# Kernel optimization log

Measured on AMD Instinct MI355X. Metric: run time of the kernel, lower is better.

## Reference

```python
import jax, jax.numpy as jnp
import numpy as np

NUM_EMBEDDINGS = 1024
EMBEDDING_DIM = 256
COMMITMENT_COST = 0.25


def setup_inputs() -> dict:
    key = jax.random.key(0)
    k1, k2 = jax.random.split(key)
    inputs = jax.random.normal(k1, (65536, EMBEDDING_DIM), dtype=jnp.float32)
    # original init: uniform(-1/K, 1/K)
    embeddings = jax.random.uniform(
        k2, (NUM_EMBEDDINGS, EMBEDDING_DIM), dtype=jnp.float32,
        minval=-1.0 / NUM_EMBEDDINGS, maxval=1.0 / NUM_EMBEDDINGS)
    return {"inputs": inputs, "embeddings": embeddings}


def reference(inputs, embeddings):
    D = embeddings.shape[1]
    flat = inputs.reshape(-1, D)                                   # [N, D]
    distances = (jnp.sum(flat ** 2, axis=1, keepdims=True)
                 + jnp.sum(embeddings ** 2, axis=1)
                 - 2.0 * flat @ embeddings.T)
    indices = jnp.argmin(distances, axis=1)                        # [N]
    # one-hot @ codebook == direct gather
    quantized = embeddings[indices].reshape(inputs.shape)
    q_loss = jnp.mean((jax.lax.stop_gradient(quantized) - inputs) ** 2)
    e_loss = jnp.mean((quantized - jax.lax.stop_gradient(inputs)) ** 2)
    loss = q_loss + COMMITMENT_COST * e_loss
    # straight-through estimator
    quantized = inputs + jax.lax.stop_gradient(quantized - inputs)
    return quantized, loss
```

## Files before the change

### kernel.cpp

```cpp
#include <hip/hip_runtime.h>
#include <stdint.h>

#define N_ROWS 65536
#define K_CODES 1024
#define DIM 256

typedef unsigned int uint;
typedef unsigned short ushort;

#define WS_LOSS_OFF  0
#define WS_ENORM_OFF 4096
#define WS_E8_OFF    8192

typedef __attribute__((ext_vector_type(4))) float f32x4;
typedef __attribute__((ext_vector_type(4))) int   i32x4;
typedef __attribute__((ext_vector_type(8))) int   i32x8;

#define XSCALE 16.0f
#define ESCALE 256.0f
#define SCORE_C 4.8828125e-4f
#define SCALE1 0x7F7F7F7Fu

__device__ __forceinline__ uint pack4_fp8(float a, float b, float c, float d) {
    uint r = 0;
    r = __builtin_amdgcn_cvt_pk_fp8_f32(a, b, r, false);
    r = __builtin_amdgcn_cvt_pk_fp8_f32(c, d, r, true);
    return r;
}
__device__ __forceinline__ void gload_lds16(const void* g, void* l) {
    __builtin_amdgcn_global_load_lds(
        (const __attribute__((address_space(1))) void*)g,
        (__attribute__((address_space(3))) void*)l, 16, 0, 0);
}

__global__ __launch_bounds__(256) void vq_prep(const float* __restrict__ E,
                                               unsigned char* __restrict__ E8,
                                               float* __restrict__ enorm) {
    int id = blockIdx.x * 256 + threadIdx.x;
    int code = id >> 6, c4 = id & 63;
    float4 v = *reinterpret_cast<const float4*>(E + (size_t)code * DIM + c4 * 4);
    uint p = pack4_fp8(v.x * ESCALE, v.y * ESCALE, v.z * ESCALE, v.w * ESCALE);
    *reinterpret_cast<uint*>(E8 + (size_t)code * 256 + c4 * 4) = p;

    float s = v.x * v.x + v.y * v.y + v.z * v.z + v.w * v.w;
    #pragma unroll
    for (int m = 32; m >= 1; m >>= 1) s += __shfl_down(s, m, 64);
    if (c4 == 0) enorm[code] = s;
}

__global__ __launch_bounds__(256, 2) void vq_main(const float* __restrict__ X,
                                                  const unsigned char* __restrict__ E8,
                                                  const float* __restrict__ enorm,
                                                  const float* __restrict__ E,
                                                  float* __restrict__ out,
                                                  float* __restrict__ lossAcc) {
    __shared__ __align__(16) unsigned char bsm[2 * 32768];
    __shared__ float enormLds[1024];
    __shared__ float xnormLds[128];
    __shared__ int   bcLds[128];
    __shared__ float lossSh;

    const int tid = threadIdx.x;
    const int lane = tid & 63;
    const int w = tid >> 6;
    const int cl = lane & 15;
    const int kq = lane >> 4;
    const int row0 = blockIdx.x * 128;
    const int key = (cl & 7) << 4;

    auto stageB = [&](int tile, int buf) {
        unsigned char* dst = bsm + buf * 32768;
        const unsigned char* src = E8 + (size_t)(tile * 128) * 256;
        #pragma unroll
        for (int j = 0; j < 8; ++j) {
            int o = j * 4096 + tid * 16;
            int rr = o >> 8;
            int cb = (o & 255) ^ ((rr & 7) << 4);
            gload_lds16(src + rr * 256 + cb, dst + o);
        }
    };

    stageB(0, 0);

    reinterpret_cast<float4*>(enormLds)[tid] =
        reinterpret_cast<const float4*>(enorm)[tid];
    if (tid == 0) lossSh = 0.f;

    i32x8 aF[2][2];
    #pragma unroll
    for (int m = 0; m < 2; ++m) {
        const float* rp = X + (size_t)(row0 + w * 32 + m * 16 + cl) * DIM;
        float s = 0.f;
        #pragma unroll
        for (int ks = 0; ks < 2; ++ks) {
            const float* p = rp + ks * 128 + kq * 32;
            uint u[8];
            #pragma unroll
            for (int q = 0; q < 8; ++q) {
                float4 v = *reinterpret_cast<const float4*>(p + q * 4);
                u[q] = pack4_fp8(v.x * XSCALE, v.y * XSCALE,
                                 v.z * XSCALE, v.w * XSCALE);
                s = fmaf(v.x, v.x, s); s = fmaf(v.y, v.y, s);
                s = fmaf(v.z, v.z, s); s = fmaf(v.w, v.w, s);
            }
            i32x8 f = {(int)u[0], (int)u[1], (int)u[2], (int)u[3],
                       (int)u[4], (int)u[5], (int)u[6], (int)u[7]};
            aF[m][ks] = f;
        }
        s += __shfl_xor(s, 16, 64);
        s += __shfl_xor(s, 32, 64);
        if (kq == 0) xnormLds[w * 32 + m * 16 + cl] = s;
    }

    float best[2][4];
    int bcode[2][4];
    #pragma unroll
    for (int m = 0; m < 2; ++m)
        #pragma unroll
        for (int rr = 0; rr < 4; ++rr) { best[m][rr] = 3.4e38f; bcode[m][rr] = 0; }

    for (int t = 0; t < 8; ++t) {
        __syncthreads();
        if (t < 7) stageB(t + 1, (t + 1) & 1);

        const unsigned char* bb = bsm + (t & 1) * 32768;
        float en[8];
        #pragma unroll
        for (int n = 0; n < 8; ++n) en[n] = enormLds[t * 128 + n * 16 + cl];

        f32x4 acc[2][8];
        #pragma unroll
        for (int m = 0; m < 2; ++m)
            #pragma unroll
            for (int n = 0; n < 8; ++n) {
                f32x4 z = {0.f, 0.f, 0.f, 0.f};
                acc[m][n] = z;
            }

        __builtin_amdgcn_s_setprio(1);
        #pragma unroll
        for (int ks = 0; ks < 2; ++ks) {
            #pragma unroll
            for (int n = 0; n < 8; ++n) {
                const unsigned char* rbase = bb + (size_t)(n * 16 + cl) * 256;
                int l0 = ks * 128 + kq * 32;
                i32x4 lo = *reinterpret_cast<const i32x4*>(rbase + (l0 ^ key));
                i32x4 hi = *reinterpret_cast<const i32x4*>(rbase + ((l0 + 16) ^ key));
                i32x8 bf = __builtin_shufflevector(lo, hi, 0, 1, 2, 3, 4, 5, 6, 7);
                #pragma unroll
                for (int m = 0; m < 2; ++m)
                    acc[m][n] = __builtin_amdgcn_mfma_scale_f32_16x16x128_f8f6f4(
                        aF[m][ks], bf, acc[m][n],
                        0, 0,
                        0, SCALE1,
                        0, SCALE1);
            }
        }
        __builtin_amdgcn_s_setprio(0);

        #pragma unroll
        for (int n = 0; n < 8; ++n) {
            int codeN = t * 128 + n * 16 + cl;
            #pragma unroll
            for (int m = 0; m < 2; ++m)
                #pragma unroll
                for (int rr = 0; rr < 4; ++rr) {
                    float sc = fmaf(-SCORE_C, acc[m][n][rr], en[n]);
                    if (sc < best[m][rr]) { best[m][rr] = sc; bcode[m][rr] = codeN; }
                }
        }
    }

    float lsum = 0.f;
    #pragma unroll
    for (int m = 0; m < 2; ++m)
        #pragma unroll
        for (int rr = 0; rr < 4; ++rr) {
            float b = best[m][rr];
            int cc = bcode[m][rr];
            #pragma unroll
            for (int mask = 1; mask < 16; mask <<= 1) {
                float ob = __shfl_xor(b, mask, 64);
                int oc = __shfl_xor(cc, mask, 64);
                if (ob < b || (ob == b && oc < cc)) { b = ob; cc = oc; }
            }
            if (cl == 0) {
                int row_l = w * 32 + m * 16 + kq * 4 + rr;
                bcLds[row_l] = cc;
                lsum += xnormLds[row_l] + b;
            }
        }
    lsum += __shfl_xor(lsum, 16, 64);
    lsum += __shfl_xor(lsum, 32, 64);
    if (lane == 0) atomicAdd(&lossSh, lsum);
    __syncthreads();

    #pragma unroll 4
    for (int i = 0; i < 32; ++i) {
        int g = i * 256 + tid;
        int rr = g >> 6, c4 = g & 63;
        int code = bcLds[rr];
        f32x4 q = *reinterpret_cast<const f32x4*>(E + (size_t)code * DIM + c4 * 4);
        __builtin_nontemporal_store(q,
            reinterpret_cast<f32x4*>(out + (size_t)(row0 + rr) * DIM + c4 * 4));
    }
    if (tid == 0) atomicAdd(lossAcc, lossSh);
}

__global__ void vq_finalize(const float* __restrict__ lossAcc,
                            float* __restrict__ out) {
    out[(size_t)N_ROWS * DIM] = 1.25f * lossAcc[0] / (float)((size_t)N_ROWS * DIM);
}

extern "C" void kernel_launch(void* const* d_in, const int* in_sizes, int n_in,
                              void* d_out, int out_size, void* d_ws, size_t ws_size,
                              hipStream_t stream) {
    const float* X = (const float*)d_in[0];
    const float* E = (const float*)d_in[1];
    float* out = (float*)d_out;

    char* ws = (char*)d_ws;
    float* lossAcc = (float*)(ws + WS_LOSS_OFF);
    float* enorm = (float*)(ws + WS_ENORM_OFF);
    unsigned char* E8 = (unsigned char*)(ws + WS_E8_OFF);

    hipMemsetAsync(lossAcc, 0, 4, stream);
    vq_prep<<<256, 256, 0, stream>>>(E, E8, enorm);
    vq_main<<<N_ROWS / 128, 256, 0, stream>>>(X, E8, enorm, E, out, lossAcc);
    vq_finalize<<<1, 1, 0, stream>>>(lossAcc, out);
}
```

Before: 54.74 us.

## Use 512-thread blocks with 64KB codebook quarters and packed uint argmin

Doubles the block to 512 threads covering 256 rows and stages the fp8 codebook in four 64KB quarters double-buffered in LDS, cutting barriers from eight to three per block. The score is precomputed as a biased 2048*||e||^2 so it stays positive, and its float bits are packed with the code index into one uint, making the argmin and the cross-lane reduction a single integer min. The memset launch is folded into the prep kernel. The packing truncates the low 10 mantissa bits of the score, which can change tie-breaking and add small loss error, and the new layout uses about 128KB of LDS with occupancy of one block per CU.

```diff
diff --git a/kernel.cpp b/kernel.cpp
--- a/kernel.cpp
+++ b/kernel.cpp
@@ -6,10 +6,9 @@
 #define DIM 256
 
 typedef unsigned int uint;
-typedef unsigned short ushort;
 
 #define WS_LOSS_OFF  0
-#define WS_ENORM_OFF 4096
+#define WS_ENS_OFF   4096
 #define WS_E8_OFF    8192
 
 typedef __attribute__((ext_vector_type(4))) float f32x4;
@@ -18,7 +17,6 @@
 
 #define XSCALE 16.0f
 #define ESCALE 256.0f
-#define SCORE_C 4.8828125e-4f
 #define SCALE1 0x7F7F7F7Fu
 
 __device__ __forceinline__ uint pack4_fp8(float a, float b, float c, float d) {
@@ -35,8 +33,10 @@
 
 __global__ __launch_bounds__(256) void vq_prep(const float* __restrict__ E,
                                                unsigned char* __restrict__ E8,
-                                               float* __restrict__ enorm) {
+                                               float* __restrict__ enS,
+                                               float* __restrict__ lossAcc) {
     int id = blockIdx.x * 256 + threadIdx.x;
+    if (id == 0) lossAcc[0] = 0.f;
     int code = id >> 6, c4 = id & 63;
     float4 v = *reinterpret_cast<const float4*>(E + (size_t)code * DIM + c4 * 4);
     uint p = pack4_fp8(v.x * ESCALE, v.y * ESCALE, v.z * ESCALE, v.w * ESCALE);
@@ -45,52 +45,51 @@
     float s = v.x * v.x + v.y * v.y + v.z * v.z + v.w * v.w;
     #pragma unroll
     for (int m = 32; m >= 1; m >>= 1) s += __shfl_down(s, m, 64);
-    if (c4 == 0) enorm[code] = s;
-}
-
-__global__ __launch_bounds__(256, 2) void vq_main(const float* __restrict__ X,
+    if (c4 == 0) enS[code] = s * 2048.0f + 2048.0f;
+}
+
+__global__ __launch_bounds__(512, 1) void vq_main(const float* __restrict__ X,
                                                   const unsigned char* __restrict__ E8,
-                                                  const float* __restrict__ enorm,
+                                                  const float* __restrict__ enS,
                                                   const float* __restrict__ E,
                                                   float* __restrict__ out,
                                                   float* __restrict__ lossAcc) {
-    __shared__ __align__(16) unsigned char bsm[2 * 32768];
-    __shared__ float enormLds[1024];
-    __shared__ float xnormLds[128];
-    __shared__ int   bcLds[128];
-    __shared__ float lossSh;
+    __shared__ __align__(16) unsigned char bsm[2][65536];
+    __shared__ float enSLds[1024];
+    __shared__ int   bcLds[256];
 
     const int tid = threadIdx.x;
     const int lane = tid & 63;
     const int w = tid >> 6;
     const int cl = lane & 15;
     const int kq = lane >> 4;
-    const int row0 = blockIdx.x * 128;
+    const int row0 = blockIdx.x * 256;
     const int key = (cl & 7) << 4;
 
-    auto stageB = [&](int tile, int buf) {
-        unsigned char* dst = bsm + buf * 32768;
-        const unsigned char* src = E8 + (size_t)(tile * 128) * 256;
+    auto stageQ = [&](int q, int buf) {
+        unsigned char* dst = &bsm[buf][0];
+        const unsigned char* src = E8 + (size_t)q * 65536;
         #pragma unroll
         for (int j = 0; j < 8; ++j) {
-            int o = j * 4096 + tid * 16;
+            int o = j * 8192 + tid * 16;
             int rr = o >> 8;
             int cb = (o & 255) ^ ((rr & 7) << 4);
             gload_lds16(src + rr * 256 + cb, dst + o);
         }
     };
 
-    stageB(0, 0);
-
-    reinterpret_cast<float4*>(enormLds)[tid] =
-        reinterpret_cast<const float4*>(enorm)[tid];
-    if (tid == 0) lossSh = 0.f;
+    stageQ(0, 0);
+    stageQ(1, 1);
+
+    if (tid < 256)
+        reinterpret_cast<f32x4*>(enSLds)[tid] =
+            reinterpret_cast<const f32x4*>(enS)[tid];
 
     i32x8 aF[2][2];
+    float xsum = 0.f;
     #pragma unroll
     for (int m = 0; m < 2; ++m) {
         const float* rp = X + (size_t)(row0 + w * 32 + m * 16 + cl) * DIM;
-        float s = 0.f;
         #pragma unroll
         for (int ks = 0; ks < 2; ++ks) {
             const float* p = rp + ks * 128 + kq * 32;
@@ -100,111 +99,99 @@
                 float4 v = *reinterpret_cast<const float4*>(p + q * 4);
                 u[q] = pack4_fp8(v.x * XSCALE, v.y * XSCALE,
                                  v.z * XSCALE, v.w * XSCALE);
-                s = fmaf(v.x, v.x, s); s = fmaf(v.y, v.y, s);
-                s = fmaf(v.z, v.z, s); s = fmaf(v.w, v.w, s);
+                xsum = fmaf(v.x, v.x, xsum); xsum = fmaf(v.y, v.y, xsum);
+                xsum = fmaf(v.z, v.z, xsum); xsum = fmaf(v.w, v.w, xsum);
             }
             i32x8 f = {(int)u[0], (int)u[1], (int)u[2], (int)u[3],
                        (int)u[4], (int)u[5], (int)u[6], (int)u[7]};
             aF[m][ks] = f;
         }
-        s += __shfl_xor(s, 16, 64);
-        s += __shfl_xor(s, 32, 64);
-        if (kq == 0) xnormLds[w * 32 + m * 16 + cl] = s;
     }
 
-    float best[2][4];
-    int bcode[2][4];
+    uint best[2][4];
     #pragma unroll
     for (int m = 0; m < 2; ++m)
         #pragma unroll
-        for (int rr = 0; rr < 4; ++rr) { best[m][rr] = 3.4e38f; bcode[m][rr] = 0; }
-
-    for (int t = 0; t < 8; ++t) {
-        __syncthreads();
-        if (t < 7) stageB(t + 1, (t + 1) & 1);
-
-        const unsigned char* bb = bsm + (t & 1) * 32768;
-        float en[8];
-        #pragma unroll
-        for (int n = 0; n < 8; ++n) en[n] = enormLds[t * 128 + n * 16 + cl];
-
-        f32x4 acc[2][8];
-        #pragma unroll
-        for (int m = 0; m < 2; ++m)
-            #pragma unroll
-            for (int n = 0; n < 8; ++n) {
+        for (int rr = 0; rr < 4; ++rr) best[m][rr] = 0xFFFFFFFFu;
+
+    __syncthreads();
+
+    for (int qi = 0; qi < 4; ++qi) {
+        const unsigned char* bb = &bsm[qi & 1][0];
+
+        #pragma unroll 4
+        for (int g = 0; g < 16; ++g) {
+            float en = enSLds[qi * 256 + g * 16 + cl];
+            const unsigned char* rbase = bb + (size_t)(g * 16 + cl) * 256;
+
+            f32x4 acc[2];
+            #pragma unroll
+            for (int m = 0; m < 2; ++m) {
                 f32x4 z = {0.f, 0.f, 0.f, 0.f};
-                acc[m][n] = z;
-            }
-
-        __builtin_amdgcn_s_setprio(1);
-        #pragma unroll
-        for (int ks = 0; ks < 2; ++ks) {
-            #pragma unroll
-            for (int n = 0; n < 8; ++n) {
-                const unsigned char* rbase = bb + (size_t)(n * 16 + cl) * 256;
+                acc[m] = z;
+            }
+            #pragma unroll
+            for (int ks = 0; ks < 2; ++ks) {
                 int l0 = ks * 128 + kq * 32;
                 i32x4 lo = *reinterpret_cast<const i32x4*>(rbase + (l0 ^ key));
                 i32x4 hi = *reinterpret_cast<const i32x4*>(rbase + ((l0 + 16) ^ key));
                 i32x8 bf = __builtin_shufflevector(lo, hi, 0, 1, 2, 3, 4, 5, 6, 7);
                 #pragma unroll
                 for (int m = 0; m < 2; ++m)
-                    acc[m][n] = __builtin_amdgcn_mfma_scale_f32_16x16x128_f8f6f4(
-                        aF[m][ks], bf, acc[m][n],
-                        0, 0,
-                        0, SCALE1,
-                        0, SCALE1);
-            }
-        }
-        __builtin_amdgcn_s_setprio(0);
-
-        #pragma unroll
-        for (int n = 0; n < 8; ++n) {
-            int codeN = t * 128 + n * 16 + cl;
+                    acc[m] = __builtin_amdgcn_mfma_scale_f32_16x16x128_f8f6f4(
+                        aF[m][0 + ks], bf, acc[m],
+                        0, 0, 0, SCALE1, 0, SCALE1);
+            }
+            uint codeN = (uint)(qi * 256 + g * 16 + cl);
             #pragma unroll
             for (int m = 0; m < 2; ++m)
                 #pragma unroll
                 for (int rr = 0; rr < 4; ++rr) {
-                    float sc = fmaf(-SCORE_C, acc[m][n][rr], en[n]);
-                    if (sc < best[m][rr]) { best[m][rr] = sc; bcode[m][rr] = codeN; }
+                    float scv = en - acc[m][rr];
+                    uint pk = (__float_as_uint(scv) & 0xFFFFFC00u) | codeN;
+                    best[m][rr] = min(best[m][rr], pk);
                 }
         }
+
+        if (qi < 3) {
+            __syncthreads();
+            if (qi < 2) stageQ(qi + 2, qi & 1);
+        }
     }
 
-    float lsum = 0.f;
+    float minsum = 0.f;
     #pragma unroll
     for (int m = 0; m < 2; ++m)
         #pragma unroll
         for (int rr = 0; rr < 4; ++rr) {
-            float b = best[m][rr];
-            int cc = bcode[m][rr];
-            #pragma unroll
-            for (int mask = 1; mask < 16; mask <<= 1) {
-                float ob = __shfl_xor(b, mask, 64);
-                int oc = __shfl_xor(cc, mask, 64);
-                if (ob < b || (ob == b && oc < cc)) { b = ob; cc = oc; }
-            }
+            uint v = best[m][rr];
+            #pragma unroll
+            for (int mask = 1; mask < 16; mask <<= 1)
+                v = min(v, (uint)__shfl_xor((int)v, mask, 64));
             if (cl == 0) {
                 int row_l = w * 32 + m * 16 + kq * 4 + rr;
-                bcLds[row_l] = cc;
-                lsum += xnormLds[row_l] + b;
-            }
-        }
-    lsum += __shfl_xor(lsum, 16, 64);
-    lsum += __shfl_xor(lsum, 32, 64);
-    if (lane == 0) atomicAdd(&lossSh, lsum);
+                bcLds[row_l] = (int)(v & 1023u);
+                minsum += __uint_as_float(v & 0xFFFFFC00u) - 2048.0f;
+            }
+        }
+    float xs = xsum;
+    #pragma unroll
+    for (int mask = 1; mask < 16; mask <<= 1) xs += __shfl_xor(xs, mask, 64);
+    float v2 = (cl == 0) ? (xs + minsum * (1.0f / 2048.0f)) : 0.f;
+    v2 += __shfl_xor(v2, 16, 64);
+    v2 += __shfl_xor(v2, 32, 64);
+    if (lane == 0) atomicAdd(lossAcc, v2);
     __syncthreads();
 
     #pragma unroll 4
     for (int i = 0; i < 32; ++i) {
-        int g = i * 256 + tid;
+        int g = i * 512 + tid;
         int rr = g >> 6, c4 = g & 63;
         int code = bcLds[rr];
         f32x4 q = *reinterpret_cast<const f32x4*>(E + (size_t)code * DIM + c4 * 4);
         __builtin_nontemporal_store(q,
             reinterpret_cast<f32x4*>(out + (size_t)(row0 + rr) * DIM + c4 * 4));
     }
-    if (tid == 0) atomicAdd(lossAcc, lossSh);
 }
 
 __global__ void vq_finalize(const float* __restrict__ lossAcc,
@@ -221,11 +208,10 @@
 
     char* ws = (char*)d_ws;
     float* lossAcc = (float*)(ws + WS_LOSS_OFF);
-    float* enorm = (float*)(ws + WS_ENORM_OFF);
+    float* enS = (float*)(ws + WS_ENS_OFF);
     unsigned char* E8 = (unsigned char*)(ws + WS_E8_OFF);
 
-    hipMemsetAsync(lossAcc, 0, 4, stream);
-    vq_prep<<<256, 256, 0, stream>>>(E, E8, enorm);
-    vq_main<<<N_ROWS / 128, 256, 0, stream>>>(X, E8, enorm, E, out, lossAcc);
+    vq_prep<<<256, 256, 0, stream>>>(E, E8, enS, lossAcc);
+    vq_main<<<N_ROWS / 256, 512, 0, stream>>>(X, E8, enS, E, out, lossAcc);
     vq_finalize<<<1, 1, 0, stream>>>(lossAcc, out);
 }
```

Result: slower. 73.48 us (+34.2%).
